# Performance work log

Measured on AMD Instinct MI355X. Metric: run time of the kernel, lower is better.

Reference implementation:

```python
import jax, jax.numpy as jnp
import numpy as np

B, NPG, D, E = 64, 1024, 128, 524288
N = B * NPG
K1, K2, K3 = 820, 656, 525  # ceil(0.8*1024), ceil(0.8*820), ceil(0.8*656)
VOCAB = 100000
EPS = 1e-5


def setup_inputs() -> dict:
    key = jax.random.key(0)
    ks = jax.random.split(key, 16)
    epg = E // B
    off = jnp.repeat(jnp.arange(B, dtype=jnp.int32) * NPG, epg)
    src = jax.random.randint(ks[0], (E,), 0, NPG, dtype=jnp.int32) + off
    dst = jax.random.randint(ks[1], (E,), 0, NPG, dtype=jnp.int32) + off
    edge_index = jnp.stack([src, dst])  # [2, E], within-graph edges
    node_idx = jax.random.randint(ks[2], (N, 1), 0, VOCAB, dtype=jnp.int32)
    def lin(k, o, i):
        return jax.random.normal(k, (o, i), jnp.float32) / np.sqrt(i).astype(np.float32)
    return dict(
        node_idx=node_idx, edge_index=edge_index,
        emb=jax.random.normal(ks[3], (VOCAB, D), jnp.float32),
        w1l=lin(ks[4], 128, D), b1l=jnp.zeros(128, jnp.float32), w1r=lin(ks[5], 128, D),
        pool_w=jax.random.normal(ks[6], (128,), jnp.float32) / np.float32(np.sqrt(128)),
        w2l=lin(ks[7], 128, 128), b2l=jnp.zeros(128, jnp.float32), w2r=lin(ks[8], 128, 128),
        fc1_w=lin(ks[9], 128, 256), fc1_b=jnp.zeros(128, jnp.float32),
        bn1_g=jnp.ones(128, jnp.float32), bn1_b=jnp.zeros(128, jnp.float32),
        fc2_w=lin(ks[10], 64, 128), fc2_b=jnp.zeros(64, jnp.float32),
        bn2_g=jnp.ones(64, jnp.float32), bn2_b=jnp.zeros(64, jnp.float32),
        lin_w=lin(ks[11], 1, 64), lin_b=jnp.zeros(1, jnp.float32),
    )


def _sage(x, src, dst, em, wl, bl, wr):
    # PyG SAGEConv: lin_l(mean_{j->i} x_j) + lin_r(x_i); em masks dropped edges
    n = x.shape[0]
    s = jax.ops.segment_sum(x[src] * em[:, None], dst, num_segments=n)
    c = jax.ops.segment_sum(em, dst, num_segments=n)
    mean = s / jnp.maximum(c, 1.0)[:, None]
    return mean @ wl.T + bl + x @ wr.T


def _topk(x, src, dst, em, w, k):
    # PyG TopKPooling: score = x.w/||w||, per-graph top-k, gate by tanh(score)
    n = x.shape[0]
    npg = n // B
    score = (x @ w) / jnp.linalg.norm(w)
    vals, idx = jax.lax.top_k(score.reshape(B, npg), k)  # [B,k]
    perm = (idx + (jnp.arange(B, dtype=idx.dtype) * npg)[:, None]).reshape(-1)
    xn = x[perm] * jnp.tanh(vals).reshape(-1)[:, None]
    new_id = jnp.full((n,), -1, jnp.int32).at[perm].set(jnp.arange(B * k, dtype=jnp.int32))
    ns, nd = new_id[src], new_id[dst]
    em2 = em * (ns >= 0) * (nd >= 0)  # keep only edges with both endpoints kept
    return xn, jnp.maximum(ns, 0), jnp.maximum(nd, 0), em2


def _readout(x, k):
    # global_max_pool || global_mean_pool (graphs are contiguous, size k)
    xr = x.reshape(B, k, -1)
    return jnp.concatenate([xr.max(axis=1), xr.mean(axis=1)], axis=1)


def _bn(x, g, b):
    m = x.mean(0)
    v = jnp.mean((x - m) ** 2, axis=0)  # biased var, as in BatchNorm1d training
    return (x - m) / jnp.sqrt(v + EPS) * g + b


def reference(node_idx, edge_index, emb, w1l, b1l, w1r, pool_w,
              w2l, b2l, w2r, fc1_w, fc1_b, bn1_g, bn1_b,
              fc2_w, fc2_b, bn2_g, bn2_b, lin_w, lin_b):
    src, dst = edge_index[0], edge_index[1]
    em = jnp.ones((E,), jnp.float32)
    x = emb[node_idx[:, 0]]                                   # [N,128]
    x = jax.nn.relu(_sage(x, src, dst, em, w1l, b1l, w1r))
    x, src, dst, em = _topk(x, src, dst, em, pool_w, K1)
    x1 = _readout(x, K1)
    x = jax.nn.relu(_sage(x, src, dst, em, w2l, b2l, w2r))
    x, src, dst, em = _topk(x, src, dst, em, pool_w, K2)
    x2 = _readout(x, K2)
    x = jax.nn.relu(_sage(x, src, dst, em, w2l, b2l, w2r))
    x, src, dst, em = _topk(x, src, dst, em, pool_w, K3)
    x3 = _readout(x, K3)
    h = x1 + x2 + x3                                          # [B,256]
    h = jax.nn.relu(_bn(h @ fc1_w.T + fc1_b, bn1_g, bn1_b))
    h = jax.nn.relu(_bn(h @ fc2_w.T + fc2_b, bn2_g, bn2_b))
    # dropout is identity in eval mode
    return jax.nn.sigmoid(h @ lin_w.T + lin_b)[:, 0]          # [B]
```

## Files before the change

### kernel.cpp

```cpp
#include <hip/hip_runtime.h>
#include <hip/hip_bf16.h>
#include <cstdint>
#include <cstddef>

#define NGRAPH 64
#define NPG0   1024
#define NNODE  65536
#define NEDGE  524288
#define EPG    8192
#define DIM    128
#define RCHUNK 16

typedef __attribute__((ext_vector_type(8))) short short8v;
typedef __attribute__((ext_vector_type(4))) float f32x4;

__device__ __forceinline__ unsigned bf16rne(float f) {
  unsigned u = __float_as_uint(f);
  return (u + 0x7FFFu + ((u >> 16) & 1u)) >> 16;
}

__global__ __launch_bounds__(256) void k_gather(const float* __restrict__ emb,
    const int* __restrict__ nid, float* __restrict__ x)
{
  int tid = blockIdx.x * 256 + threadIdx.x;
  int i = tid >> 5, lane = tid & 31;
  int row = nid[i];
  ((float4*)(x + (size_t)i * DIM))[lane] =
      ((const float4*)(emb + (size_t)row * DIM))[lane];
}

__global__ __launch_bounds__(64) void k_norm(const float* __restrict__ pw,
    float* __restrict__ inv_norm)
{
  int t = threadIdx.x;
  float a = pw[t], b = pw[t + 64];
  float v = a * a + b * b;
  for (int off = 32; off; off >>= 1) v += __shfl_xor(v, off);
  if (t == 0) *inv_norm = 1.0f / sqrtf(v);
}

__global__ __launch_bounds__(256) void k_prep_wfrag(
    const float* __restrict__ w1l, const float* __restrict__ w1r,
    const float* __restrict__ w2l, const float* __restrict__ w2r,
    short* __restrict__ whiF, short* __restrict__ wloF)
{
  int id = blockIdx.x * 256 + threadIdx.x;
  int set = id >> 15;
  int r = id & 32767;
  int j  = r & 7;
  int l  = (r >> 3) & 63;
  int nt = (r >> 9) & 7;
  int kk = r >> 12;
  int k = kk * 32 + ((l >> 4) & 3) * 8 + j;
  int n = nt * 16 + (l & 15);
  const float* wl = set ? w2l : w1l;
  const float* wr = set ? w2r : w1r;
  float w = (k < 128) ? wl[n * 128 + k] : wr[n * 128 + (k - 128)];
  unsigned hb = bf16rne(w);
  float hif = __uint_as_float(hb << 16);
  unsigned lb = bf16rne(w - hif);
  whiF[id] = (short)hb;
  wloF[id] = (short)lb;
}

__global__ __launch_bounds__(1024) void k_csr0(const int* __restrict__ ei,
    int* __restrict__ off_g, int* __restrict__ elist_g, float* __restrict__ c_out)
{
  __shared__ int cnt[1024];
  __shared__ int cur[1024];
  __shared__ int wsum[16];
  const int t = threadIdx.x, g = blockIdx.x;
  const int nodeBase = g * NPG0;
  const int e0 = g * EPG;
  cnt[t] = 0;
  __syncthreads();
  int sv8[8], dl8[8];
  #pragma unroll
  for (int i = 0; i < 8; ++i) {
    int e = e0 + t + i * 1024;
    sv8[i] = ei[e];
    dl8[i] = ei[NEDGE + e] - nodeBase;
    atomicAdd(&cnt[dl8[i]], 1);
  }
  __syncthreads();
  const int lane = t & 63, w = t >> 6;
  int cv = cnt[t];
  int x = cv;
  #pragma unroll
  for (int off = 1; off < 64; off <<= 1) {
    int y = __shfl_up(x, off);
    if (lane >= off) x += y;
  }
  if (lane == 63) wsum[w] = x;
  __syncthreads();
  if (t < 16) {
    int v = wsum[t];
    #pragma unroll
    for (int off2 = 1; off2 < 16; off2 <<= 1) {
      int y = __shfl_up(v, off2);
      if (t >= off2) v += y;
    }
    wsum[t] = v;
  }
  __syncthreads();
  int incl = x + (w ? wsum[w - 1] : 0);
  int excl = incl - cv;
  cur[t] = excl;
  int* offp = off_g + g * 1025;
  offp[t] = excl;
  if (t == 1023) offp[1024] = incl;
  c_out[nodeBase + t] = (float)cv;
  __syncthreads();
  int* elp = elist_g + g * EPG;
  #pragma unroll
  for (int i = 0; i < 8; ++i) {
    int pos = atomicAdd(&cur[dl8[i]], 1);
    elp[pos] = sv8[i];
  }
}

__global__ __launch_bounds__(256) void k_agg_gemm(
    const int* __restrict__ off_g, const int* __restrict__ elist_g,
    const float* __restrict__ x, float* __restrict__ h_out,
    const short* __restrict__ whiF, const short* __restrict__ wloF,
    const float* __restrict__ bl, const float* __restrict__ pw,
    float* __restrict__ score, int npg)
{
  __shared__ float sA[64 * 128];
  __shared__ float cntA[64];
  const int g     = blockIdx.x & 63;
  const int slice = blockIdx.x >> 6;
  const int nodeBase = g * npg;
  const int vbase = slice * 64;
  const int t = threadIdx.x;

  {
    const int gr = t >> 5, l32 = t & 31;
    const int* off = off_g + g * 1025;
    const int* el  = elist_g + g * EPG;
    #pragma unroll
    for (int i = 0; i < 8; ++i) {
      int vb = gr * 8 + i;
      int v = vbase + vb;
      float4 acc = {0.f, 0.f, 0.f, 0.f};
      int cn = 0;
      if (v < npg) {
        int e = off[v], end = off[v + 1];
        cn = end - e;
        for (; e + 4 <= end; e += 4) {
          int s0 = el[e], s1 = el[e + 1], s2 = el[e + 2], s3 = el[e + 3];
          float4 a0 = ((const float4*)(x + (size_t)s0 * DIM))[l32];
          float4 a1 = ((const float4*)(x + (size_t)s1 * DIM))[l32];
          float4 a2 = ((const float4*)(x + (size_t)s2 * DIM))[l32];
          float4 a3 = ((const float4*)(x + (size_t)s3 * DIM))[l32];
          acc.x += (a0.x + a1.x) + (a2.x + a3.x);
          acc.y += (a0.y + a1.y) + (a2.y + a3.y);
          acc.z += (a0.z + a1.z) + (a2.z + a3.z);
          acc.w += (a0.w + a1.w) + (a2.w + a3.w);
        }
        for (; e + 2 <= end; e += 2) {
          int s0 = el[e], s1 = el[e + 1];
          float4 a0 = ((const float4*)(x + (size_t)s0 * DIM))[l32];
          float4 a1 = ((const float4*)(x + (size_t)s1 * DIM))[l32];
          acc.x += a0.x + a1.x; acc.y += a0.y + a1.y;
          acc.z += a0.z + a1.z; acc.w += a0.w + a1.w;
        }
        if (e < end) {
          float4 a = ((const float4*)(x + (size_t)el[e] * DIM))[l32];
          acc.x += a.x; acc.y += a.y; acc.z += a.z; acc.w += a.w;
        }
      }
      ((float4*)(sA + vb * 128))[l32] = acc;
      if (l32 == 0) cntA[vb] = (float)cn;
    }
  }
  __syncthreads();

  const int wv = t >> 6, l = t & 63;
  const int lrow = l & 15, lk = l >> 4;
  const int rb = wv * 16;
  const int rowb = rb + lrow;
  const int rowg = nodeBase + min(vbase + rowb, npg - 1);
  const float invc = 1.0f / fmaxf(cntA[rowb], 1.0f);
  f32x4 acc[8];
  #pragma unroll
  for (int nt = 0; nt < 8; ++nt) acc[nt] = (f32x4){0.f, 0.f, 0.f, 0.f};
  const float* srow = sA + rowb * 128 + lk * 8;
  const float* xrow = x + (size_t)rowg * DIM + lk * 8;
  const short8v* bh = (const short8v*)whiF;
  const short8v* bo = (const short8v*)wloF;

  #pragma unroll
  for (int kk = 0; kk < 8; ++kk) {
    float av[8];
    if (kk < 4) {
      float4 a0 = *(const float4*)(srow + kk * 32);
      float4 a1 = *(const float4*)(srow + kk * 32 + 4);
      av[0] = a0.x * invc; av[1] = a0.y * invc;
      av[2] = a0.z * invc; av[3] = a0.w * invc;
      av[4] = a1.x * invc; av[5] = a1.y * invc;
      av[6] = a1.z * invc; av[7] = a1.w * invc;
    } else {
      float4 a0 = *(const float4*)(xrow + (kk - 4) * 32);
      float4 a1 = *(const float4*)(xrow + (kk - 4) * 32 + 4);
      av[0] = a0.x; av[1] = a0.y; av[2] = a0.z; av[3] = a0.w;
      av[4] = a1.x; av[5] = a1.y; av[6] = a1.z; av[7] = a1.w;
    }
    short8v ahi, alo;
    #pragma unroll
    for (int j = 0; j < 8; ++j) {
      unsigned hb = bf16rne(av[j]);
      float hif = __uint_as_float(hb << 16);
      ahi[j] = (short)hb;
      alo[j] = (short)bf16rne(av[j] - hif);
    }
    #pragma unroll
    for (int nt = 0; nt < 8; ++nt) {
      int fi = (kk * 8 + nt) * 64 + l;
      short8v bhi = bh[fi];
      short8v blo = bo[fi];
      acc[nt] = __builtin_amdgcn_mfma_f32_16x16x32_bf16(ahi, bhi, acc[nt], 0, 0, 0);
      acc[nt] = __builtin_amdgcn_mfma_f32_16x16x32_bf16(alo, bhi, acc[nt], 0, 0, 0);
      acc[nt] = __builtin_amdgcn_mfma_f32_16x16x32_bf16(ahi, blo, acc[nt], 0, 0, 0);
    }
  }

  float sp0 = 0.f, sp1 = 0.f, sp2 = 0.f, sp3 = 0.f;
  const int mbv = vbase + rb + lk * 4;
  #pragma unroll
  for (int nt = 0; nt < 8; ++nt) {
    int col = nt * 16 + lrow;
    float bb = bl[col], pv = pw[col];
    float h0 = fmaxf(acc[nt][0] + bb, 0.f);
    float h1 = fmaxf(acc[nt][1] + bb, 0.f);
    float h2 = fmaxf(acc[nt][2] + bb, 0.f);
    float h3 = fmaxf(acc[nt][3] + bb, 0.f);
    if (mbv + 0 < npg) h_out[(size_t)(nodeBase + mbv + 0) * DIM + col] = h0;
    if (mbv + 1 < npg) h_out[(size_t)(nodeBase + mbv + 1) * DIM + col] = h1;
    if (mbv + 2 < npg) h_out[(size_t)(nodeBase + mbv + 2) * DIM + col] = h2;
    if (mbv + 3 < npg) h_out[(size_t)(nodeBase + mbv + 3) * DIM + col] = h3;
    sp0 += h0 * pv; sp1 += h1 * pv; sp2 += h2 * pv; sp3 += h3 * pv;
  }
  #pragma unroll
  for (int off = 1; off <= 8; off <<= 1) {
    sp0 += __shfl_xor(sp0, off);
    sp1 += __shfl_xor(sp1, off);
    sp2 += __shfl_xor(sp2, off);
    sp3 += __shfl_xor(sp3, off);
  }
  if (lrow == 0) {
    if (mbv + 0 < npg) score[nodeBase + mbv + 0] = sp0;
    if (mbv + 1 < npg) score[nodeBase + mbv + 1] = sp1;
    if (mbv + 2 < npg) score[nodeBase + mbv + 2] = sp2;
    if (mbv + 3 < npg) score[nodeBase + mbv + 3] = sp3;
  }
}

__global__ __launch_bounds__(1024) void k_topk_fused(
    const float* __restrict__ score, const float* __restrict__ inv_norm_p,
    int npg, int k, int* __restrict__ sel_pos, float* __restrict__ sel_scale,
    int build_next, int write_eout,
    const int* __restrict__ ein_src, const int* __restrict__ ein_dst,
    int* __restrict__ eout_src, int* __restrict__ eout_dst,
    int* __restrict__ off_g, int* __restrict__ elist_g, float* __restrict__ c_out)
{
  __shared__ float key[1024];
  __shared__ int   idxs[1024];
  __shared__ int   nid[1024];
  __shared__ int   cnt[1024];
  __shared__ int   cur[1024];
  __shared__ int   wsum[16];
  const int t = threadIdx.x, g = blockIdx.x;
  const int base = g * npg;
  key[t] = (t < npg) ? score[base + t] : -3.402823466e38f;
  idxs[t] = t;
  nid[t] = -1;
  cnt[t] = 0;
  __syncthreads();
  for (int size = 2; size <= 1024; size <<= 1) {
    for (int stride = size >> 1; stride > 0; stride >>= 1) {
      int p = t ^ stride;
      if (p > t) {
        float ka = key[t], kb = key[p];
        int ia = idxs[t], ib = idxs[p];
        bool a_first = (ka > kb) || (ka == kb && ia < ib);
        bool desc = ((t & size) == 0);
        if (desc ? !a_first : a_first) {
          key[t] = kb; key[p] = ka; idxs[t] = ib; idxs[p] = ia;
        }
      }
      __syncthreads();
    }
  }
  if (t < k) {
    float inv = *inv_norm_p;
    int local = idxs[t];
    nid[local] = t;
    sel_pos[g * k + t] = base + local;
    sel_scale[g * k + t] = tanhf(key[t] * inv);
  }
  if (!build_next) return;
  __syncthreads();
  const int e0 = g * EPG;
  const int newBase = g * k;
  int lns[8], lnd[8];
  #pragma unroll
  for (int i = 0; i < 8; ++i) {
    int e = e0 + t + i * 1024;
    int sv = ein_src[e];
    int ns = -1, nd = -1;
    if (sv >= 0) {
      int dv = ein_dst[e];
      ns = nid[sv - base];
      nd = nid[dv - base];
      if (ns < 0 || nd < 0) ns = -1;
    }
    lns[i] = ns; lnd[i] = nd;
    if (write_eout) {
      eout_src[e] = (ns >= 0) ? (newBase + ns) : -1;
      eout_dst[e] = (ns >= 0) ? (newBase + nd) : -1;
    }
    if (ns >= 0) atomicAdd(&cnt[nd], 1);
  }
  __syncthreads();
  const int lane = t & 63, w = t >> 6;
  int cv = cnt[t];
  int x = cv;
  #pragma unroll
  for (int off = 1; off < 64; off <<= 1) {
    int y = __shfl_up(x, off);
    if (lane >= off) x += y;
  }
  if (lane == 63) wsum[w] = x;
  __syncthreads();
  if (t < 16) {
    int v = wsum[t];
    #pragma unroll
    for (int off2 = 1; off2 < 16; off2 <<= 1) {
      int y = __shfl_up(v, off2);
      if (t >= off2) v += y;
    }
    wsum[t] = v;
  }
  __syncthreads();
  int incl = x + (w ? wsum[w - 1] : 0);
  int excl = incl - cv;
  cur[t] = excl;
  off_g[g * 1025 + t] = excl;
  if (t < k) c_out[newBase + t] = (float)cv;
  __syncthreads();
  int* elp = elist_g + g * EPG;
  #pragma unroll
  for (int i = 0; i < 8; ++i) {
    if (lns[i] >= 0) {
      int pos = atomicAdd(&cur[lnd[i]], 1);
      elp[pos] = newBase + lns[i];
    }
  }
}

__global__ __launch_bounds__(256) void k_pool_part(const float* __restrict__ h,
    const int* __restrict__ sel_pos, const float* __restrict__ sel_scale, int k,
    float* __restrict__ xo, float* __restrict__ pmax, float* __restrict__ psum)
{
  __shared__ float4 smx[256], ssm[256];
  const int b  = blockIdx.x >> 4;
  const int ch = blockIdx.x & (RCHUNK - 1);
  const int rpc = (k + RCHUNK - 1) / RCHUNK;
  const int r0 = ch * rpc;
  const int r1 = min(k, r0 + rpc);
  const int d4  = threadIdx.x & 31;
  const int sub = threadIdx.x >> 5;
  const float NEG = -3.402823466e38f;
  float4 mx = {NEG, NEG, NEG, NEG};
  float4 sm = {0.f, 0.f, 0.f, 0.f};
  for (int r = r0 + sub; r < r1; r += 8) {
    int j = b * k + r;
    float scv = sel_scale[j];
    float4 v = ((const float4*)(h + (size_t)sel_pos[j] * DIM))[d4];
    v.x *= scv; v.y *= scv; v.z *= scv; v.w *= scv;
    ((float4*)(xo + (size_t)j * DIM))[d4] = v;
    mx.x = fmaxf(mx.x, v.x); mx.y = fmaxf(mx.y, v.y);
    mx.z = fmaxf(mx.z, v.z); mx.w = fmaxf(mx.w, v.w);
    sm.x += v.x; sm.y += v.y; sm.z += v.z; sm.w += v.w;
  }
  smx[threadIdx.x] = mx; ssm[threadIdx.x] = sm;
  __syncthreads();
  if (sub < 4) {
    #pragma unroll
    for (int step = 4; step >= 1; step >>= 1) {
      if (sub < step) {
        float4 m2 = smx[(sub + step) * 32 + d4];
        float4 s2 = ssm[(sub + step) * 32 + d4];
        mx = smx[sub * 32 + d4]; sm = ssm[sub * 32 + d4];
        mx.x = fmaxf(mx.x, m2.x); mx.y = fmaxf(mx.y, m2.y);
        mx.z = fmaxf(mx.z, m2.z); mx.w = fmaxf(mx.w, m2.w);
        sm.x += s2.x; sm.y += s2.y; sm.z += s2.z; sm.w += s2.w;
        smx[sub * 32 + d4] = mx; ssm[sub * 32 + d4] = sm;
      }
      __syncthreads();
    }
  }
  if (sub == 0) {
    int o = (b * RCHUNK + ch) * 32 + d4;
    ((float4*)pmax)[o] = smx[d4];
    ((float4*)psum)[o] = ssm[d4];
  }
}

__global__ __launch_bounds__(128) void k_readout_final(const float* __restrict__ pmax,
    const float* __restrict__ psum, int k, float* __restrict__ rdT, int add)
{
  int b = blockIdx.x, d = threadIdx.x;
  float mx = -3.402823466e38f, sm = 0.f;
  #pragma unroll
  for (int c = 0; c < RCHUNK; ++c) {
    int o = (b * RCHUNK + c) * 128 + d;
    mx = fmaxf(mx, pmax[o]);
    sm += psum[o];
  }
  float mean = sm / (float)k;
  int omx = d * 64 + b;
  int omn = (128 + d) * 64 + b;
  if (add) { rdT[omx] += mx; rdT[omn] += mean; }
  else     { rdT[omx]  = mx; rdT[omn]  = mean; }
}

__global__ __launch_bounds__(512) void k_mlp_fc1(const float* __restrict__ rdT,
    const float* __restrict__ fc1_w, const float* __restrict__ fc1_b,
    const float* __restrict__ g1, const float* __restrict__ be1,
    float* __restrict__ y1n)
{
  __shared__ float W[8 * 256];
  __shared__ float R[256 * 64];
  const int t = threadIdx.x, b = blockIdx.x;
  ((float4*)W)[t] = ((const float4*)(fc1_w + (size_t)b * 8 * 256))[t];
  #pragma unroll
  for (int i = 0; i < 8; ++i)
    ((float4*)R)[t + i * 512] = ((const float4*)rdT)[t + i * 512];
  __syncthreads();
  const int g = t & 63, w = t >> 6;
  const float* wrow = W + w * 256;
  float acc = 0.f;
  #pragma unroll 4
  for (int k = 0; k < 256; ++k) acc += R[k * 64 + g] * wrow[k];
  int f = b * 8 + w;
  float y = acc + fc1_b[f];
  float s = y, s2 = y * y;
  #pragma unroll
  for (int off = 32; off; off >>= 1) {
    s  += __shfl_xor(s,  off);
    s2 += __shfl_xor(s2, off);
  }
  float mu = s * 0.015625f;
  float var = s2 * 0.015625f - mu * mu;
  float inv = 1.0f / sqrtf(var + 1e-5f);
  y1n[f * 64 + g] = fmaxf((y - mu) * inv * g1[f] + be1[f], 0.f);
}

__global__ __launch_bounds__(1024) void k_mlp_rest(const float* __restrict__ y1n,
    const float* __restrict__ fc2_w, const float* __restrict__ fc2_b,
    const float* __restrict__ g2, const float* __restrict__ be2,
    const float* __restrict__ lin_w, const float* __restrict__ lin_b,
    float* __restrict__ out)
{
  __shared__ float W2[64 * 128];
  __shared__ float Y[128 * 64];
  __shared__ float part[16 * 64];
  const int t = threadIdx.x;
  #pragma unroll
  for (int i = 0; i < 2; ++i) {
    ((float4*)W2)[t + i * 1024] = ((const float4*)fc2_w)[t + i * 1024];
    ((float4*)Y) [t + i * 1024] = ((const float4*)y1n)[t + i * 1024];
  }
  __syncthreads();
  const int g = t & 63, w = t >> 6;
  float acc2[4] = {0.f, 0.f, 0.f, 0.f};
  const float* w20 = W2 + (w * 4 + 0) * 128;
  const float* w21 = W2 + (w * 4 + 1) * 128;
  const float* w22 = W2 + (w * 4 + 2) * 128;
  const float* w23 = W2 + (w * 4 + 3) * 128;
  #pragma unroll 4
  for (int k = 0; k < 128; ++k) {
    float yv = Y[k * 64 + g];
    acc2[0] += yv * w20[k];
    acc2[1] += yv * w21[k];
    acc2[2] += yv * w22[k];
    acc2[3] += yv * w23[k];
  }
  float pp = 0.f;
  #pragma unroll
  for (int j = 0; j < 4; ++j) {
    int m = w * 4 + j;
    float y = acc2[j] + fc2_b[m];
    float s = y, s2 = y * y;
    #pragma unroll
    for (int off = 32; off; off >>= 1) {
      s  += __shfl_xor(s,  off);
      s2 += __shfl_xor(s2, off);
    }
    float mu = s * 0.015625f;
    float var = s2 * 0.015625f - mu * mu;
    float inv = 1.0f / sqrtf(var + 1e-5f);
    float yn = fmaxf((y - mu) * inv * g2[m] + be2[m], 0.f);
    pp += yn * lin_w[m];
  }
  part[w * 64 + g] = pp;
  __syncthreads();
  if (w == 0) {
    float a = lin_b[0];
    #pragma unroll
    for (int c = 0; c < 16; ++c) a += part[c * 64 + g];
    out[g] = 1.0f / (1.0f + expf(-a));
  }
}

extern "C" void kernel_launch(void* const* d_in, const int* in_sizes, int n_in,
                              void* d_out, int out_size, void* d_ws, size_t ws_size,
                              hipStream_t stream) {
  const int*   node_idx = (const int*)  d_in[0];
  const int*   edge_idx = (const int*)  d_in[1];
  const float* emb      = (const float*)d_in[2];
  const float* w1l      = (const float*)d_in[3];
  const float* b1l      = (const float*)d_in[4];
  const float* w1r      = (const float*)d_in[5];
  const float* pool_w   = (const float*)d_in[6];
  const float* w2l      = (const float*)d_in[7];
  const float* b2l      = (const float*)d_in[8];
  const float* w2r      = (const float*)d_in[9];
  const float* fc1_w    = (const float*)d_in[10];
  const float* fc1_b    = (const float*)d_in[11];
  const float* bn1_g    = (const float*)d_in[12];
  const float* bn1_b    = (const float*)d_in[13];
  const float* fc2_w    = (const float*)d_in[14];
  const float* fc2_b    = (const float*)d_in[15];
  const float* bn2_g    = (const float*)d_in[16];
  const float* bn2_b    = (const float*)d_in[17];
  const float* lin_w    = (const float*)d_in[18];
  const float* lin_b    = (const float*)d_in[19];
  float* out = (float*)d_out;

  char* p = (char*)d_ws;
  auto alloc = [&](size_t bytes) -> void* {
    void* r = (void*)p;
    p += (bytes + 255) & ~(size_t)255;
    return r;
  };
  float* x_cur     = (float*)alloc((size_t)NNODE * DIM * 4);
  float* s_buf     = (float*)alloc((size_t)NNODE * DIM * 4);
  float* c_buf     = (float*)alloc((size_t)NNODE * 4);
  float* score     = (float*)alloc((size_t)NNODE * 4);
  int*   sel_pos   = (int*)  alloc((size_t)NGRAPH * 820 * 4);
  float* sel_scale = (float*)alloc((size_t)NGRAPH * 820 * 4);
  int*   src_cur   = (int*)  alloc((size_t)NEDGE * 4);
  int*   dst_cur   = (int*)  alloc((size_t)NEDGE * 4);
  int*   off_g     = (int*)  alloc((size_t)NGRAPH * 1025 * 4);
  int*   elist_g   = (int*)  alloc((size_t)NGRAPH * EPG * 4);
  float* rdT       = (float*)alloc((size_t)256 * 64 * 4);
  short* whiF      = (short*)alloc((size_t)2 * 32768 * 2);
  short* wloF      = (short*)alloc((size_t)2 * 32768 * 2);
  float* y1n       = (float*)alloc((size_t)128 * 64 * 4);
  float* pmax      = (float*)alloc((size_t)NGRAPH * RCHUNK * 128 * 4);
  float* psum      = (float*)alloc((size_t)NGRAPH * RCHUNK * 128 * 4);
  float* inv_norm  = (float*)alloc(256);

  k_gather<<<NNODE * 32 / 256, 256, 0, stream>>>(emb, node_idx, x_cur);
  k_norm<<<1, 64, 0, stream>>>(pool_w, inv_norm);
  k_prep_wfrag<<<256, 256, 0, stream>>>(w1l, w1r, w2l, w2r, whiF, wloF);
  k_csr0<<<NGRAPH, 1024, 0, stream>>>(edge_idx, off_g, elist_g, c_buf);

  const int Ks[3] = {820, 656, 525};
  int npg = NPG0;
  for (int stage = 0; stage < 3; ++stage) {
    const short* whi_s = whiF + (stage ? 32768 : 0);
    const short* wlo_s = wloF + (stage ? 32768 : 0);
    const float* bl    = stage ? b2l : b1l;
    int k = Ks[stage];
    int slices = (npg + 63) >> 6;

    k_agg_gemm<<<slices * 64, 256, 0, stream>>>(off_g, elist_g, x_cur, s_buf,
                                                whi_s, wlo_s, bl, pool_w,
                                                score, npg);
    const int* ein_s = (stage == 0) ? edge_idx          : src_cur;
    const int* ein_d = (stage == 0) ? (edge_idx + NEDGE) : dst_cur;
    k_topk_fused<<<NGRAPH, 1024, 0, stream>>>(score, inv_norm, npg, k,
        sel_pos, sel_scale,
        (stage < 2) ? 1 : 0, (stage == 0) ? 1 : 0,
        ein_s, ein_d, src_cur, dst_cur,
        off_g, elist_g, c_buf);
    k_pool_part<<<NGRAPH * RCHUNK, 256, 0, stream>>>(s_buf, sel_pos, sel_scale, k,
                                                     x_cur, pmax, psum);
    k_readout_final<<<NGRAPH, 128, 0, stream>>>(pmax, psum, k, rdT, stage == 0 ? 0 : 1);
    npg = k;
  }

  k_mlp_fc1<<<16, 512, 0, stream>>>(rdT, fc1_w, fc1_b, bn1_g, bn1_b, y1n);
  k_mlp_rest<<<1, 1024, 0, stream>>>(y1n, fc2_w, fc2_b, bn2_g, bn2_b,
                                     lin_w, lin_b, out);
}
```

Measured before the change: 277.3 us.

## Split aggregation into LDS-staged planar CSC kernel and separate MFMA GEMM

Node features are stored in a per-graph planar layout of 16-float planes, so each block can stage one plane of a whole graph (up to 64KB) in LDS. Neighbor aggregation then reads from LDS instead of doing random global gathers. Edge lists switch to graph-local indices to make this work. The fused aggregation+GEMM kernel is split into two kernels with an extra h buffer, which adds a launch and a round trip of the aggregated sums through global memory.

```diff
diff --git a/kernel.cpp b/kernel.cpp
--- a/kernel.cpp
+++ b/kernel.cpp
@@ -11,6 +11,7 @@
 #define DIM    128
 #define RCHUNK 16
 
+
 typedef __attribute__((ext_vector_type(8))) short short8v;
 typedef __attribute__((ext_vector_type(4))) float f32x4;
 
@@ -25,8 +26,10 @@
   int tid = blockIdx.x * 256 + threadIdx.x;
   int i = tid >> 5, lane = tid & 31;
   int row = nid[i];
-  ((float4*)(x + (size_t)i * DIM))[lane] =
-      ((const float4*)(emb + (size_t)row * DIM))[lane];
+  float4 v = ((const float4*)(emb + (size_t)row * DIM))[lane];
+  int g = i >> 10, vl = i & 1023;
+  int p = lane >> 2, o = lane & 3;
+  ((float4*)(x + (size_t)g * NPG0 * 128 + (size_t)p * NPG0 * 16 + (size_t)vl * 16))[o] = v;
 }
 
 __global__ __launch_bounds__(64) void k_norm(const float* __restrict__ pw,
@@ -78,7 +81,7 @@
   #pragma unroll
   for (int i = 0; i < 8; ++i) {
     int e = e0 + t + i * 1024;
-    sv8[i] = ei[e];
+    sv8[i] = ei[e] - nodeBase;
     dl8[i] = ei[NEDGE + e] - nodeBase;
     atomicAdd(&cnt[dl8[i]], 1);
   }
@@ -119,93 +122,82 @@
   }
 }
 
-__global__ __launch_bounds__(256) void k_agg_gemm(
+__global__ __launch_bounds__(512) void k_csc_agg(
     const int* __restrict__ off_g, const int* __restrict__ elist_g,
-    const float* __restrict__ x, float* __restrict__ h_out,
+    const float* __restrict__ x, float* __restrict__ s, int npg)
+{
+  __shared__ float xs[16384];
+  const int g = blockIdx.x & 63;
+  const int p = blockIdx.x >> 6;
+  const int t = threadIdx.x;
+  const size_t pb = (size_t)g * npg * 128 + (size_t)p * npg * 16;
+  const float4* xp4 = (const float4*)(x + pb);
+  const int n4 = npg * 4;
+  for (int i = t; i < n4; i += 512) ((float4*)xs)[i] = xp4[i];
+  __syncthreads();
+  const int grp = t >> 4, l16 = t & 15;
+  const int per = (npg + 31) >> 5;
+  const int v0 = grp * per;
+  const int v1 = min(npg, v0 + per);
+  const int* off = off_g + g * 1025;
+  const int* el  = elist_g + g * EPG;
+  float* sp = s + pb;
+  for (int v = v0; v < v1; ++v) {
+    int e = off[v], end = off[v + 1];
+    float acc = 0.f;
+    for (; e + 8 <= end; e += 8) {
+      int s0 = el[e+0], s1 = el[e+1], s2 = el[e+2], s3 = el[e+3];
+      int s4 = el[e+4], s5 = el[e+5], s6 = el[e+6], s7 = el[e+7];
+      acc += ((xs[s0*16+l16] + xs[s1*16+l16]) + (xs[s2*16+l16] + xs[s3*16+l16]))
+           + ((xs[s4*16+l16] + xs[s5*16+l16]) + (xs[s6*16+l16] + xs[s7*16+l16]));
+    }
+    for (; e + 2 <= end; e += 2) {
+      int s0 = el[e], s1 = el[e+1];
+      acc += xs[s0*16+l16] + xs[s1*16+l16];
+    }
+    if (e < end) acc += xs[el[e]*16 + l16];
+    sp[v * 16 + l16] = acc;
+  }
+}
+
+__global__ __launch_bounds__(256) void k_gemm_plane(
+    const float* __restrict__ x, const float* __restrict__ s,
+    const float* __restrict__ c, float* __restrict__ h_out,
     const short* __restrict__ whiF, const short* __restrict__ wloF,
     const float* __restrict__ bl, const float* __restrict__ pw,
     float* __restrict__ score, int npg)
 {
-  __shared__ float sA[64 * 128];
-  __shared__ float cntA[64];
-  const int g     = blockIdx.x & 63;
+  const int g = blockIdx.x & 63;
   const int slice = blockIdx.x >> 6;
   const int nodeBase = g * npg;
   const int vbase = slice * 64;
   const int t = threadIdx.x;
-
-  {
-    const int gr = t >> 5, l32 = t & 31;
-    const int* off = off_g + g * 1025;
-    const int* el  = elist_g + g * EPG;
-    #pragma unroll
-    for (int i = 0; i < 8; ++i) {
-      int vb = gr * 8 + i;
-      int v = vbase + vb;
-      float4 acc = {0.f, 0.f, 0.f, 0.f};
-      int cn = 0;
-      if (v < npg) {
-        int e = off[v], end = off[v + 1];
-        cn = end - e;
-        for (; e + 4 <= end; e += 4) {
-          int s0 = el[e], s1 = el[e + 1], s2 = el[e + 2], s3 = el[e + 3];
-          float4 a0 = ((const float4*)(x + (size_t)s0 * DIM))[l32];
-          float4 a1 = ((const float4*)(x + (size_t)s1 * DIM))[l32];
-          float4 a2 = ((const float4*)(x + (size_t)s2 * DIM))[l32];
-          float4 a3 = ((const float4*)(x + (size_t)s3 * DIM))[l32];
-          acc.x += (a0.x + a1.x) + (a2.x + a3.x);
-          acc.y += (a0.y + a1.y) + (a2.y + a3.y);
-          acc.z += (a0.z + a1.z) + (a2.z + a3.z);
-          acc.w += (a0.w + a1.w) + (a2.w + a3.w);
-        }
-        for (; e + 2 <= end; e += 2) {
-          int s0 = el[e], s1 = el[e + 1];
-          float4 a0 = ((const float4*)(x + (size_t)s0 * DIM))[l32];
-          float4 a1 = ((const float4*)(x + (size_t)s1 * DIM))[l32];
-          acc.x += a0.x + a1.x; acc.y += a0.y + a1.y;
-          acc.z += a0.z + a1.z; acc.w += a0.w + a1.w;
-        }
-        if (e < end) {
-          float4 a = ((const float4*)(x + (size_t)el[e] * DIM))[l32];
-          acc.x += a.x; acc.y += a.y; acc.z += a.z; acc.w += a.w;
-        }
-      }
-      ((float4*)(sA + vb * 128))[l32] = acc;
-      if (l32 == 0) cntA[vb] = (float)cn;
-    }
-  }
-  __syncthreads();
-
   const int wv = t >> 6, l = t & 63;
   const int lrow = l & 15, lk = l >> 4;
-  const int rb = wv * 16;
-  const int rowb = rb + lrow;
-  const int rowg = nodeBase + min(vbase + rowb, npg - 1);
-  const float invc = 1.0f / fmaxf(cntA[rowb], 1.0f);
+  const int rowb = wv * 16 + lrow;
+  const int vclamp = min(vbase + rowb, npg - 1);
+  const float invc = 1.0f / fmaxf(c[nodeBase + vclamp], 1.0f);
+  const size_t gb = (size_t)g * npg * 128;
+  const size_t pstride = (size_t)npg * 16;
+  const int po = (lk & 1) * 8;
+  const int ph = lk >> 1;
+  const float* sbase = s + gb + (size_t)vclamp * 16 + po;
+  const float* xbase = x + gb + (size_t)vclamp * 16 + po;
   f32x4 acc[8];
   #pragma unroll
   for (int nt = 0; nt < 8; ++nt) acc[nt] = (f32x4){0.f, 0.f, 0.f, 0.f};
-  const float* srow = sA + rowb * 128 + lk * 8;
-  const float* xrow = x + (size_t)rowg * DIM + lk * 8;
   const short8v* bh = (const short8v*)whiF;
   const short8v* bo = (const short8v*)wloF;
 
   #pragma unroll
   for (int kk = 0; kk < 8; ++kk) {
-    float av[8];
-    if (kk < 4) {
-      float4 a0 = *(const float4*)(srow + kk * 32);
-      float4 a1 = *(const float4*)(srow + kk * 32 + 4);
-      av[0] = a0.x * invc; av[1] = a0.y * invc;
-      av[2] = a0.z * invc; av[3] = a0.w * invc;
-      av[4] = a1.x * invc; av[5] = a1.y * invc;
-      av[6] = a1.z * invc; av[7] = a1.w * invc;
-    } else {
-      float4 a0 = *(const float4*)(xrow + (kk - 4) * 32);
-      float4 a1 = *(const float4*)(xrow + (kk - 4) * 32 + 4);
-      av[0] = a0.x; av[1] = a0.y; av[2] = a0.z; av[3] = a0.w;
-      av[4] = a1.x; av[5] = a1.y; av[6] = a1.z; av[7] = a1.w;
-    }
+    const float* ap = (kk < 4) ? (sbase + (size_t)(kk * 2 + ph) * pstride)
+                               : (xbase + (size_t)((kk - 4) * 2 + ph) * pstride);
+    float scl = (kk < 4) ? invc : 1.0f;
+    float4 a0 = *(const float4*)ap;
+    float4 a1 = *(const float4*)(ap + 4);
+    float av[8] = { a0.x * scl, a0.y * scl, a0.z * scl, a0.w * scl,
+                    a1.x * scl, a1.y * scl, a1.z * scl, a1.w * scl };
     short8v ahi, alo;
     #pragma unroll
     for (int j = 0; j < 8; ++j) {
@@ -226,7 +218,7 @@
   }
 
   float sp0 = 0.f, sp1 = 0.f, sp2 = 0.f, sp3 = 0.f;
-  const int mbv = vbase + rb + lk * 4;
+  const int mbv = vbase + wv * 16 + lk * 4;
   #pragma unroll
   for (int nt = 0; nt < 8; ++nt) {
     int col = nt * 16 + lrow;
@@ -354,7 +346,7 @@
   for (int i = 0; i < 8; ++i) {
     if (lns[i] >= 0) {
       int pos = atomicAdd(&cur[lnd[i]], 1);
-      elp[pos] = newBase + lns[i];
+      elp[pos] = lns[i];
     }
   }
 }
@@ -371,6 +363,8 @@
   const int r1 = min(k, r0 + rpc);
   const int d4  = threadIdx.x & 31;
   const int sub = threadIdx.x >> 5;
+  const int pl = d4 >> 2, o4 = d4 & 3;
+  const size_t xgb = (size_t)b * k * 128;
   const float NEG = -3.402823466e38f;
   float4 mx = {NEG, NEG, NEG, NEG};
   float4 sm = {0.f, 0.f, 0.f, 0.f};
@@ -379,7 +373,7 @@
     float scv = sel_scale[j];
     float4 v = ((const float4*)(h + (size_t)sel_pos[j] * DIM))[d4];
     v.x *= scv; v.y *= scv; v.z *= scv; v.w *= scv;
-    ((float4*)(xo + (size_t)j * DIM))[d4] = v;
+    ((float4*)(xo + xgb + (size_t)pl * k * 16 + (size_t)r * 16))[o4] = v;
     mx.x = fmaxf(mx.x, v.x); mx.y = fmaxf(mx.y, v.y);
     mx.z = fmaxf(mx.z, v.z); mx.w = fmaxf(mx.w, v.w);
     sm.x += v.x; sm.y += v.y; sm.z += v.z; sm.w += v.w;
@@ -548,6 +542,7 @@
   };
   float* x_cur     = (float*)alloc((size_t)NNODE * DIM * 4);
   float* s_buf     = (float*)alloc((size_t)NNODE * DIM * 4);
+  float* h_buf     = (float*)alloc((size_t)NNODE * DIM * 4);
   float* c_buf     = (float*)alloc((size_t)NNODE * 4);
   float* score     = (float*)alloc((size_t)NNODE * 4);
   int*   sel_pos   = (int*)  alloc((size_t)NGRAPH * 820 * 4);
@@ -578,9 +573,10 @@
     int k = Ks[stage];
     int slices = (npg + 63) >> 6;
 
-    k_agg_gemm<<<slices * 64, 256, 0, stream>>>(off_g, elist_g, x_cur, s_buf,
-                                                whi_s, wlo_s, bl, pool_w,
-                                                score, npg);
+    k_csc_agg<<<8 * NGRAPH, 512, 0, stream>>>(off_g, elist_g, x_cur, s_buf, npg);
+    k_gemm_plane<<<slices * 64, 256, 0, stream>>>(x_cur, s_buf, c_buf, h_buf,
+                                                  whi_s, wlo_s, bl, pool_w,
+                                                  score, npg);
     const int* ein_s = (stage == 0) ? edge_idx          : src_cur;
     const int* ein_d = (stage == 0) ? (edge_idx + NEDGE) : dst_cur;
     k_topk_fused<<<NGRAPH, 1024, 0, stream>>>(score, inv_norm, npg, k,
@@ -588,7 +584,7 @@
         (stage < 2) ? 1 : 0, (stage == 0) ? 1 : 0,
         ein_s, ein_d, src_cur, dst_cur,
         off_g, elist_g, c_buf);
-    k_pool_part<<<NGRAPH * RCHUNK, 256, 0, stream>>>(s_buf, sel_pos, sel_scale, k,
+    k_pool_part<<<NGRAPH * RCHUNK, 256, 0, stream>>>(h_buf, sel_pos, sel_scale, k,
                                                      x_cur, pmax, psum);
     k_readout_final<<<NGRAPH, 128, 0, stream>>>(pmax, psum, k, rdT, stage == 0 ? 0 : 1);
     npg = k;
```

Result: slower. 346.1 us (+24.8%).
